# Performance work log

Measured on AMD Instinct MI355X. Metric: run time of the kernel, lower is better.

## Reference

```python
import jax, jax.numpy as jnp
import numpy as np

DIM = 768
N_HEADS = 12
HEAD_DIM = DIM // N_HEADS
B, S = 2, 2048


def fibonacci_mask(seq_len, causal=True):
    fibs = [1, 1]
    while fibs[-1] + fibs[-2] <= seq_len:
        fibs.append(fibs[-1] + fibs[-2])
    mask = np.zeros((seq_len, seq_len), dtype=bool)
    i = np.arange(seq_len)
    mask[i, i] = True  # self
    for f in fibs:
        rows = i[i - f >= 0]
        mask[rows, rows - f] = True
        if not causal:
            rows = i[i + f < seq_len]
            mask[rows, rows + f] = True
    return mask


def setup_inputs() -> dict:
    key = jax.random.key(0)
    k1, k2, k3, k4, k5 = jax.random.split(key, 5)
    x = jax.random.normal(k1, (B, S, DIM), dtype=jnp.float32)
    # Linear weights (torch layout: [out, in]), small init
    w_qkv = jax.random.normal(k2, (3 * DIM, DIM), dtype=jnp.float32) * (DIM ** -0.5)
    b_qkv = jax.random.normal(k3, (3 * DIM,), dtype=jnp.float32) * 0.02
    w_out = jax.random.normal(k4, (DIM, DIM), dtype=jnp.float32) * (DIM ** -0.5)
    b_out = jax.random.normal(k5, (DIM,), dtype=jnp.float32) * 0.02
    mask = jnp.asarray(fibonacci_mask(S, causal=True))  # [S,S] bool constant
    return {"x": x, "w_qkv": w_qkv, "b_qkv": b_qkv, "w_out": w_out, "b_out": b_out, "mask": mask}


def reference(x, w_qkv, b_qkv, w_out, b_out, mask):
    Bx, Sx, D = x.shape
    qkv = x @ w_qkv.T + b_qkv                                   # [B,S,3D]
    qkv = qkv.reshape(Bx, Sx, 3, N_HEADS, HEAD_DIM)
    qkv = jnp.transpose(qkv, (2, 0, 3, 1, 4))                   # [3,B,H,S,hd]
    q, k, v = qkv[0], qkv[1], qkv[2]
    scale = HEAD_DIM ** -0.5
    attn = jnp.einsum('bhqd,bhkd->bhqk', q, k) * scale          # [B,H,S,S]
    attn = jnp.where(mask[None, None], attn, -jnp.inf)
    attn = jax.nn.softmax(attn, axis=-1)
    attn = jnp.nan_to_num(attn, nan=0.0)
    out = jnp.einsum('bhqk,bhkd->bhqd', attn, v)                # [B,H,S,hd]
    out = jnp.transpose(out, (0, 2, 1, 3)).reshape(Bx, Sx, D)
    return out @ w_out.T + b_out
```

## Files before the change

kernel.cpp:

```cpp
#include <hip/hip_runtime.h>
#include <hip/hip_bf16.h>

#define DIM   768
#define NH    12
#define HD    64
#define BB    2
#define SS    2048
#define QKVN  (3 * DIM)
#define MM    (BB * SS)

typedef __attribute__((ext_vector_type(8))) short bf16x8;
typedef __attribute__((ext_vector_type(8))) short short8;
typedef __attribute__((ext_vector_type(4))) float f32x4;

__device__ __forceinline__ short f2bf(float f) {
    unsigned int u = __float_as_uint(f);
    unsigned int r = (u + 0x7FFFu + ((u >> 16) & 1u)) >> 16;
    return (short)r;
}
__device__ __forceinline__ float bf2f(short s) {
    return __uint_as_float((unsigned int)(unsigned short)s << 16);
}

__device__ __forceinline__ void gld16(const short* g, short* l) {
    __builtin_amdgcn_global_load_lds(
        (const __attribute__((address_space(1))) void*)g,
        (__attribute__((address_space(3))) void*)l, 16, 0, 0);
}

template<int N> __device__ __forceinline__ void waitvm() {
    if constexpr (N == 0) asm volatile("s_waitcnt vmcnt(0)" ::: "memory");
    else if constexpr (N == 3) asm volatile("s_waitcnt vmcnt(3)" ::: "memory");
    else if constexpr (N == 4) asm volatile("s_waitcnt vmcnt(4)" ::: "memory");
}

__global__ __launch_bounds__(256) void conv_kernel(
    const float* __restrict__ x,  short* __restrict__ xb,
    const float* __restrict__ wq, short* __restrict__ wqb,
    const float* __restrict__ wo, short* __restrict__ wob)
{
    const int nx = (MM * DIM) / 8;
    const int nq = (QKVN * DIM) / 8;
    int i8 = blockIdx.x * 256 + threadIdx.x;
    const float* src; short* dst;
    if (i8 < nx)           { src = x;  dst = xb; }
    else if (i8 < nx + nq) { i8 -= nx; src = wq; dst = wqb; }
    else                   { i8 -= nx + nq; src = wo; dst = wob; }
    const float4* p = (const float4*)src + (size_t)i8 * 2;
    float4 a = p[0], b = p[1];
    short8 r;
    r[0] = f2bf(a.x); r[1] = f2bf(a.y); r[2] = f2bf(a.z); r[3] = f2bf(a.w);
    r[4] = f2bf(b.x); r[5] = f2bf(b.y); r[6] = f2bf(b.z); r[7] = f2bf(b.w);
    *((short8*)dst + i8) = r;
}


template<int RT>
__device__ __forceinline__ void stage_op(const short* gb, int K, int k0, short* ld)
{
#pragma unroll
    for (int ii = 0; ii < RT / 64; ++ii)
        gld16(gb + (size_t)(64 * ii) * K + k0, ld + ii * 4096);
}

template<int MF, int NF>
__device__ __forceinline__ void read_frags(
    const short* lsA, const short* lsB, int arow, int brow, int kg, int sw,
    bf16x8 af[2][MF], bf16x8 bfr[2][NF])
{
#pragma unroll
    for (int kk = 0; kk < 2; ++kk) {
        const int ko = (kk * 32 + kg * 8) ^ sw;
#pragma unroll
        for (int i = 0; i < MF; ++i)
            af[kk][i] = *(const bf16x8*)&lsA[(arow + i * 16) * 64 + ko];
#pragma unroll
        for (int j = 0; j < NF; ++j)
            bfr[kk][j] = *(const bf16x8*)&lsB[(brow + j * 16) * 64 + ko];
    }
}

template<int MF, int NF>
__device__ __forceinline__ void mfma_frags(
    bf16x8 af[2][MF], bf16x8 bfr[2][NF], f32x4 acc[MF][NF])
{
#pragma unroll
    for (int kk = 0; kk < 2; ++kk)
#pragma unroll
        for (int i = 0; i < MF; ++i)
#pragma unroll
            for (int j = 0; j < NF; ++j)
                acc[i][j] = __builtin_amdgcn_mfma_f32_16x16x32_bf16(
                    af[kk][i], bfr[kk][j], acc[i][j], 0, 0, 0);
}

template<int MF, int NF, int ART, int BRT, int VC>
__device__ __forceinline__ void phase_steady(
    const short* lsA, const short* lsB, short* ldA, short* ldB,
    const short* Ab, const short* Bb, int K, int knext,
    int arow, int brow, int kg, int sw, f32x4 acc[MF][NF])
{
    bf16x8 af[2][MF], bfr[2][NF];
    read_frags<MF, NF>(lsA, lsB, arow, brow, kg, sw, af, bfr);
    asm volatile("s_waitcnt lgkmcnt(0)" ::: "memory");
    __builtin_amdgcn_s_barrier();
    stage_op<ART>(Ab, K, knext, ldA);
    stage_op<BRT>(Bb, K, knext, ldB);
    mfma_frags<MF, NF>(af, bfr, acc);
    waitvm<VC>();
    __builtin_amdgcn_s_barrier();
}

__global__ __launch_bounds__(512) void gemm_qkv_kernel(
    const short* __restrict__ A, const short* __restrict__ Bm,
    const float* __restrict__ bias, short* __restrict__ qkvh)
{
    constexpr int K = DIM, NT = 12;
    __shared__ short lsA0[8192], lsB0[8192], lsA1[8192], lsB1[8192];

    const int t    = threadIdx.x;
    const int lane = t & 63;
    const int wid  = t >> 6;
    const int wrow = wid >> 2, wcol = wid & 3;
    const int l16  = lane & 15;
    const int kg   = lane >> 4;
    const int row0 = blockIdx.y * 128;
    const int col0 = blockIdx.x * 128;

    const int srow = t >> 3;
    const int scol = ((t & 7) ^ (srow & 7)) * 8;
    const short* Ab = A  + (size_t)(row0 + srow) * K + scol;
    const short* Bb = Bm + (size_t)(col0 + srow) * K + scol;
    short* ldA0 = lsA0 + t * 8;  short* ldB0 = lsB0 + t * 8;
    short* ldA1 = lsA1 + t * 8;  short* ldB1 = lsB1 + t * 8;
    const int arow = wrow * 64 + l16;
    const int brow = wcol * 32 + l16;
    const int sw   = (l16 & 7) * 8;

    f32x4 acc[4][2];
#pragma unroll
    for (int i = 0; i < 4; ++i)
#pragma unroll
        for (int j = 0; j < 2; ++j) acc[i][j] = (f32x4){0.f, 0.f, 0.f, 0.f};

    stage_op<128>(Ab, K, 0, ldA0);
    stage_op<128>(Bb, K, 0, ldB0);
    stage_op<128>(Ab, K, 64, ldA1);
    stage_op<128>(Bb, K, 64, ldB1);
    waitvm<4>();
    __builtin_amdgcn_s_barrier();

#pragma unroll
    for (int kt = 0; kt < NT - 2; kt += 2) {
        phase_steady<4, 2, 128, 128, 4>(lsA0, lsB0, ldA0, ldB0, Ab, Bb, K,
                                        (kt + 2) * 64, arow, brow, kg, sw, acc);
        phase_steady<4, 2, 128, 128, 4>(lsA1, lsB1, ldA1, ldB1, Ab, Bb, K,
                                        (kt + 3) * 64, arow, brow, kg, sw, acc);
    }
    {
        bf16x8 af[2][4], bfr[2][2];
        read_frags<4, 2>(lsA0, lsB0, arow, brow, kg, sw, af, bfr);
        mfma_frags<4, 2>(af, bfr, acc);
        waitvm<0>();
        __builtin_amdgcn_s_barrier();
        read_frags<4, 2>(lsA1, lsB1, arow, brow, kg, sw, af, bfr);
        mfma_frags<4, 2>(af, bfr, acc);
    }

#pragma unroll
    for (int j = 0; j < 2; ++j) {
        const int col = col0 + wcol * 32 + j * 16 + l16;
        const int ty = col / DIM;
        const int hh = (col % DIM) >> 6;
        const int dd = col & 63;
        const float bv = bias[col];
        const size_t cbase = ((size_t)(ty * BB * NH) * SS) * HD;
#pragma unroll
        for (int i = 0; i < 4; ++i) {
            const int rbase = row0 + wrow * 64 + i * 16 + kg * 4;
#pragma unroll
            for (int r = 0; r < 4; ++r) {
                const int row = rbase + r;
                const int bq = row >> 11, sq = row & 2047;
                qkvh[cbase + (((size_t)(bq * NH + hh) * SS + sq) << 6) + dd] =
                    f2bf(acc[i][j][r] + bv);
            }
        }
    }
}

__global__ __launch_bounds__(512) void gemm_out_kernel(
    const short* __restrict__ A, const short* __restrict__ Bm,
    const float* __restrict__ bias, float* __restrict__ C)
{
    constexpr int K = DIM, N = DIM, NT = 12;
    __shared__ short lsA0[4096], lsB0[8192], lsA1[4096], lsB1[8192];

    const int t    = threadIdx.x;
    const int lane = t & 63;
    const int wid  = t >> 6;
    const int wrow = wid >> 2, wcol = wid & 3;
    const int l16  = lane & 15;
    const int kg   = lane >> 4;
    const int row0 = blockIdx.y * 64;
    const int col0 = blockIdx.x * 128;

    const int srow = t >> 3;
    const int scol = ((t & 7) ^ (srow & 7)) * 8;
    const short* Ab = A  + (size_t)(row0 + srow) * K + scol;
    const short* Bb = Bm + (size_t)(col0 + srow) * K + scol;
    short* ldA0 = lsA0 + t * 8;  short* ldB0 = lsB0 + t * 8;
    short* ldA1 = lsA1 + t * 8;  short* ldB1 = lsB1 + t * 8;
    const int arow = wrow * 32 + l16;
    const int brow = wcol * 32 + l16;
    const int sw   = (l16 & 7) * 8;

    f32x4 acc[2][2];
#pragma unroll
    for (int i = 0; i < 2; ++i)
#pragma unroll
        for (int j = 0; j < 2; ++j) acc[i][j] = (f32x4){0.f, 0.f, 0.f, 0.f};

    stage_op<64>(Ab, K, 0, ldA0);
    stage_op<128>(Bb, K, 0, ldB0);
    stage_op<64>(Ab, K, 64, ldA1);
    stage_op<128>(Bb, K, 64, ldB1);
    waitvm<3>();
    __builtin_amdgcn_s_barrier();

#pragma unroll
    for (int kt = 0; kt < NT - 2; kt += 2) {
        phase_steady<2, 2, 64, 128, 3>(lsA0, lsB0, ldA0, ldB0, Ab, Bb, K,
                                       (kt + 2) * 64, arow, brow, kg, sw, acc);
        phase_steady<2, 2, 64, 128, 3>(lsA1, lsB1, ldA1, ldB1, Ab, Bb, K,
                                       (kt + 3) * 64, arow, brow, kg, sw, acc);
    }
    {
        bf16x8 af[2][2], bfr[2][2];
        read_frags<2, 2>(lsA0, lsB0, arow, brow, kg, sw, af, bfr);
        mfma_frags<2, 2>(af, bfr, acc);
        waitvm<0>();
        __builtin_amdgcn_s_barrier();
        read_frags<2, 2>(lsA1, lsB1, arow, brow, kg, sw, af, bfr);
        mfma_frags<2, 2>(af, bfr, acc);
    }

#pragma unroll
    for (int j = 0; j < 2; ++j) {
        const int col = col0 + wcol * 32 + j * 16 + l16;
        const float bv = bias[col];
#pragma unroll
        for (int i = 0; i < 2; ++i) {
            const int rbase = row0 + wrow * 32 + i * 16 + kg * 4;
#pragma unroll
            for (int r = 0; r < 4; ++r)
                C[(size_t)(rbase + r) * N + col] = acc[i][j][r] + bv;
        }
    }
}

__global__ __launch_bounds__(256) void fib_attn_kernel(
    const short* __restrict__ qkvh, short* __restrict__ attn)
{
    const int idx   = blockIdx.x;
    const int j     = idx >> 3;
    const int bh    = (idx & 7) + 8 * (j >> 6);
    const int chunk = j & 63;
    const int wid   = threadIdx.x >> 6;
    const int lane  = threadIdx.x & 63;
    const int ql    = lane >> 3;
    const int c     = lane & 7;
    const int s     = chunk * 32 + wid * 8 + ql;
    const int b = bh / NH, h = bh % NH;

    constexpr size_t TYB = (size_t)BB * NH * SS * HD;
    const size_t base = ((size_t)bh * SS) << 6;
    const short* Kp = qkvh + TYB + base;
    const short* Vp = qkvh + 2 * TYB + base;

    float qv[8];
    {
        bf16x8 v = *(const bf16x8*)(qkvh + base + ((size_t)s << 6) + c * 8);
#pragma unroll
        for (int e = 0; e < 8; ++e) qv[e] = bf2f(v[e]);
    }

    constexpr int NF = 17;
    const int fib[NF] = {0, 1, 2, 3, 5, 8, 13, 21, 34, 55, 89, 144,
                         233, 377, 610, 987, 1597};
    float sc[NF];
#pragma unroll
    for (int f = 0; f < NF; ++f) {
        const bool ok = (fib[f] <= s);
        const int sk = ok ? s - fib[f] : s;
        bf16x8 kv = *(const bf16x8*)(Kp + ((size_t)sk << 6) + c * 8);
        float part = 0.f;
#pragma unroll
        for (int e = 0; e < 8; ++e) part += qv[e] * bf2f(kv[e]);
        part += __shfl_xor(part, 1, 64);
        part += __shfl_xor(part, 2, 64);
        part += __shfl_xor(part, 4, 64);
        sc[f] = ok ? part * 0.125f : -1e30f;
    }

    float mx = sc[0];
#pragma unroll
    for (int f = 1; f < NF; ++f) mx = fmaxf(mx, sc[f]);
    float den = 0.f;
#pragma unroll
    for (int f = 0; f < NF; ++f) { sc[f] = __expf(sc[f] - mx); den += sc[f]; }

    float o[8];
#pragma unroll
    for (int e = 0; e < 8; ++e) o[e] = 0.f;
#pragma unroll
    for (int f = 0; f < NF; ++f) {
        const int sk = (fib[f] <= s) ? s - fib[f] : s;
        bf16x8 vv = *(const bf16x8*)(Vp + ((size_t)sk << 6) + c * 8);
        const float w = sc[f];
#pragma unroll
        for (int e = 0; e < 8; ++e) o[e] += w * bf2f(vv[e]);
    }

    const float inv = 1.f / den;
    short8 r;
#pragma unroll
    for (int e = 0; e < 8; ++e) r[e] = f2bf(o[e] * inv);
    *(short8*)(attn + (size_t)(b * SS + s) * DIM + h * HD + c * 8) = r;
}

extern "C" void kernel_launch(void* const* d_in, const int* in_sizes, int n_in,
                              void* d_out, int out_size, void* d_ws, size_t ws_size,
                              hipStream_t stream)
{
    const float* x     = (const float*)d_in[0];
    const float* w_qkv = (const float*)d_in[1];
    const float* b_qkv = (const float*)d_in[2];
    const float* w_out = (const float*)d_in[3];
    const float* b_out = (const float*)d_in[4];
    float* out = (float*)d_out;

    short* qkvh  = (short*)d_ws;
    short* attnb = (short*)((char*)d_ws + 18874368);
    short* xb    = (short*)((char*)d_ws + 25165824);
    short* wqkvb = (short*)((char*)d_ws + 31457280);
    short* woutb = (short*)((char*)d_ws + 34996224);

    conv_kernel<<<dim3(2688, 1, 1), dim3(256, 1, 1), 0, stream>>>(
        x, xb, w_qkv, wqkvb, w_out, woutb);

    gemm_qkv_kernel<<<dim3(QKVN / 128, MM / 128, 1), dim3(512, 1, 1), 0, stream>>>(
        xb, wqkvb, b_qkv, qkvh);

    fib_attn_kernel<<<dim3(1536, 1, 1), dim3(256, 1, 1), 0, stream>>>(qkvh, attnb);

    gemm_out_kernel<<<dim3(DIM / 128, MM / 64, 1), dim3(512, 1, 1), 0, stream>>>(
        attnb, woutb, b_out, out);
}
```

Before: 59.47 us.

## Fuse fp32-to-bf16 conversion into GEMM loaders and remap block order

Removes the separate conversion kernel. Both GEMMs now load fp32 x and weights directly through registers and convert them with packed bf16 conversion instructions before writing to swizzled LDS, with loads issued one stage ahead. Block indices are remapped to 1D with a grouped ordering, likely to improve L2 reuse. This saves a launch and the bf16 intermediate round-trip, but doubles the global bytes read per GEMM tile and adds register pressure and VALU work in the main loop.

```diff
diff --git a/kernel.cpp b/kernel.cpp
--- a/kernel.cpp
+++ b/kernel.cpp
@@ -22,6 +22,18 @@
     return __uint_as_float((unsigned int)(unsigned short)s << 16);
 }
 
+__device__ __forceinline__ unsigned cvtpk(float lo, float hi) {
+    unsigned r;
+    asm("v_cvt_pk_bf16_f32 %0, %1, %2" : "=v"(r) : "v"(lo), "v"(hi));
+    return r;
+}
+__device__ __forceinline__ void wr16(short* dst, float4 a, float4 b) {
+    int4 v;
+    v.x = (int)cvtpk(a.x, a.y); v.y = (int)cvtpk(a.z, a.w);
+    v.z = (int)cvtpk(b.x, b.y); v.w = (int)cvtpk(b.z, b.w);
+    *(int4*)dst = v;
+}
+
 __device__ __forceinline__ void gld16(const short* g, short* l) {
     __builtin_amdgcn_global_load_lds(
         (const __attribute__((address_space(1))) void*)g,
@@ -30,28 +42,9 @@
 
 template<int N> __device__ __forceinline__ void waitvm() {
     if constexpr (N == 0) asm volatile("s_waitcnt vmcnt(0)" ::: "memory");
-    else if constexpr (N == 3) asm volatile("s_waitcnt vmcnt(3)" ::: "memory");
     else if constexpr (N == 4) asm volatile("s_waitcnt vmcnt(4)" ::: "memory");
-}
-
-__global__ __launch_bounds__(256) void conv_kernel(
-    const float* __restrict__ x,  short* __restrict__ xb,
-    const float* __restrict__ wq, short* __restrict__ wqb,
-    const float* __restrict__ wo, short* __restrict__ wob)
-{
-    const int nx = (MM * DIM) / 8;
-    const int nq = (QKVN * DIM) / 8;
-    int i8 = blockIdx.x * 256 + threadIdx.x;
-    const float* src; short* dst;
-    if (i8 < nx)           { src = x;  dst = xb; }
-    else if (i8 < nx + nq) { i8 -= nx; src = wq; dst = wqb; }
-    else                   { i8 -= nx + nq; src = wo; dst = wob; }
-    const float4* p = (const float4*)src + (size_t)i8 * 2;
-    float4 a = p[0], b = p[1];
-    short8 r;
-    r[0] = f2bf(a.x); r[1] = f2bf(a.y); r[2] = f2bf(a.z); r[3] = f2bf(a.w);
-    r[4] = f2bf(b.x); r[5] = f2bf(b.y); r[6] = f2bf(b.z); r[7] = f2bf(b.w);
-    *((short8*)dst + i8) = r;
+    else if constexpr (N == 5) asm volatile("s_waitcnt vmcnt(5)" ::: "memory");
+    else if constexpr (N == 8) asm volatile("s_waitcnt vmcnt(8)" ::: "memory");
 }
 
 
@@ -94,25 +87,37 @@
                     af[kk][i], bfr[kk][j], acc[i][j], 0, 0, 0);
 }
 
-template<int MF, int NF, int ART, int BRT, int VC>
-__device__ __forceinline__ void phase_steady(
-    const short* lsA, const short* lsB, short* ldA, short* ldB,
-    const short* Ab, const short* Bb, int K, int knext,
-    int arow, int brow, int kg, int sw, f32x4 acc[MF][NF])
-{
-    bf16x8 af[2][MF], bfr[2][NF];
-    read_frags<MF, NF>(lsA, lsB, arow, brow, kg, sw, af, bfr);
-    asm volatile("s_waitcnt lgkmcnt(0)" ::: "memory");
-    __builtin_amdgcn_s_barrier();
-    stage_op<ART>(Ab, K, knext, ldA);
-    stage_op<BRT>(Bb, K, knext, ldB);
-    mfma_frags<MF, NF>(af, bfr, acc);
-    waitvm<VC>();
+template<bool ISSUE, bool WRITE, int VC>
+__device__ __forceinline__ void g1_phase(
+    const short* lsRA, const short* lsRB, short* lsWA, short* lsWB,
+    const float* Ag, const float* Bg, int knext,
+    float4* sI, const float4* sW, int wr0, int wr1,
+    int arow, int brow, int kg, int sw, f32x4 acc[4][2])
+{
+    bf16x8 af[2][4], bfr[2][2];
+    read_frags<4, 2>(lsRA, lsRB, arow, brow, kg, sw, af, bfr);
+    asm volatile("s_waitcnt lgkmcnt(0)" ::: "memory");
+    __builtin_amdgcn_s_barrier();
+    if (ISSUE) {
+#pragma unroll
+        for (int w = 0; w < 4; ++w) sI[w]     = *(const float4*)(Ag + knext + w * 4);
+#pragma unroll
+        for (int w = 0; w < 4; ++w) sI[4 + w] = *(const float4*)(Bg + knext + w * 4);
+    }
+    if (WRITE) {
+        waitvm<VC>();
+        wr16((short*)lsWA + wr0, sW[0], sW[1]);
+        wr16((short*)lsWA + wr1, sW[2], sW[3]);
+        wr16((short*)lsWB + wr0, sW[4], sW[5]);
+        wr16((short*)lsWB + wr1, sW[6], sW[7]);
+    }
+    mfma_frags<4, 2>(af, bfr, acc);
+    asm volatile("s_waitcnt lgkmcnt(0)" ::: "memory");
     __builtin_amdgcn_s_barrier();
 }
 
 __global__ __launch_bounds__(512) void gemm_qkv_kernel(
-    const short* __restrict__ A, const short* __restrict__ Bm,
+    const float* __restrict__ A, const float* __restrict__ Bm,
     const float* __restrict__ bias, short* __restrict__ qkvh)
 {
     constexpr int K = DIM, NT = 12;
@@ -124,15 +129,19 @@
     const int wrow = wid >> 2, wcol = wid & 3;
     const int l16  = lane & 15;
     const int kg   = lane >> 4;
-    const int row0 = blockIdx.y * 128;
-    const int col0 = blockIdx.x * 128;
-
-    const int srow = t >> 3;
-    const int scol = ((t & 7) ^ (srow & 7)) * 8;
-    const short* Ab = A  + (size_t)(row0 + srow) * K + scol;
-    const short* Bb = Bm + (size_t)(col0 + srow) * K + scol;
-    short* ldA0 = lsA0 + t * 8;  short* ldB0 = lsB0 + t * 8;
-    short* ldA1 = lsA1 + t * 8;  short* ldB1 = lsB1 + t * 8;
+
+    const int bid = blockIdx.x;
+    const int jj  = bid >> 3;
+    const int row0 = ((bid & 7) * 4 + jj / 18) * 128;
+    const int col0 = (jj % 18) * 128;
+
+    const int srow = t >> 2;
+    const int sc4  = (t & 3) * 16;
+    const float* Ag = A  + (size_t)(row0 + srow) * K + sc4;
+    const float* Bg = Bm + (size_t)(col0 + srow) * K + sc4;
+    const int wr0 = srow * 64 + ((((t & 3) * 2 + 0) ^ (srow & 7)) * 8);
+    const int wr1 = srow * 64 + ((((t & 3) * 2 + 1) ^ (srow & 7)) * 8);
+
     const int arow = wrow * 64 + l16;
     const int brow = wcol * 32 + l16;
     const int sw   = (l16 & 7) * 8;
@@ -143,26 +152,34 @@
 #pragma unroll
         for (int j = 0; j < 2; ++j) acc[i][j] = (f32x4){0.f, 0.f, 0.f, 0.f};
 
-    stage_op<128>(Ab, K, 0, ldA0);
-    stage_op<128>(Bb, K, 0, ldB0);
-    stage_op<128>(Ab, K, 64, ldA1);
-    stage_op<128>(Bb, K, 64, ldB1);
-    waitvm<4>();
-    __builtin_amdgcn_s_barrier();
-
-#pragma unroll
-    for (int kt = 0; kt < NT - 2; kt += 2) {
-        phase_steady<4, 2, 128, 128, 4>(lsA0, lsB0, ldA0, ldB0, Ab, Bb, K,
-                                        (kt + 2) * 64, arow, brow, kg, sw, acc);
-        phase_steady<4, 2, 128, 128, 4>(lsA1, lsB1, ldA1, ldB1, Ab, Bb, K,
-                                        (kt + 3) * 64, arow, brow, kg, sw, acc);
-    }
+    float4 s0[8], s1[8];
+#pragma unroll
+    for (int w = 0; w < 4; ++w) s0[w]     = *(const float4*)(Ag + 0 + w * 4);
+#pragma unroll
+    for (int w = 0; w < 4; ++w) s0[4 + w] = *(const float4*)(Bg + 0 + w * 4);
+#pragma unroll
+    for (int w = 0; w < 4; ++w) s1[w]     = *(const float4*)(Ag + 64 + w * 4);
+#pragma unroll
+    for (int w = 0; w < 4; ++w) s1[4 + w] = *(const float4*)(Bg + 64 + w * 4);
+    waitvm<8>();
+    wr16(lsA0 + wr0, s0[0], s0[1]);
+    wr16(lsA0 + wr1, s0[2], s0[3]);
+    wr16(lsB0 + wr0, s0[4], s0[5]);
+    wr16(lsB0 + wr1, s0[6], s0[7]);
+    asm volatile("s_waitcnt lgkmcnt(0)" ::: "memory");
+    __builtin_amdgcn_s_barrier();
+
+#pragma unroll
+    for (int kt = 0; kt < 10; kt += 2) {
+        g1_phase<true, true, 8>(lsA0, lsB0, lsA1, lsB1, Ag, Bg, (kt + 2) * 64,
+                                s0, s1, wr0, wr1, arow, brow, kg, sw, acc);
+        g1_phase<true, true, 8>(lsA1, lsB1, lsA0, lsB0, Ag, Bg, (kt + 3) * 64,
+                                s1, s0, wr0, wr1, arow, brow, kg, sw, acc);
+    }
+    g1_phase<false, true, 0>(lsA0, lsB0, lsA1, lsB1, Ag, Bg, 0,
+                             s0, s1, wr0, wr1, arow, brow, kg, sw, acc);
     {
         bf16x8 af[2][4], bfr[2][2];
-        read_frags<4, 2>(lsA0, lsB0, arow, brow, kg, sw, af, bfr);
-        mfma_frags<4, 2>(af, bfr, acc);
-        waitvm<0>();
-        __builtin_amdgcn_s_barrier();
         read_frags<4, 2>(lsA1, lsB1, arow, brow, kg, sw, af, bfr);
         mfma_frags<4, 2>(af, bfr, acc);
     }
@@ -189,11 +206,37 @@
     }
 }
 
+template<bool ISSUE, bool WRITE, int VC>
+__device__ __forceinline__ void g2_phase(
+    const short* lsRA, const short* lsRB, short* lsWB,
+    const short* Agb, const float* Bg, int knext, short* ldA,
+    float4* sI, const float4* sW, int wr0, int wr1,
+    int arow, int brow, int kg, int sw, f32x4 acc[2][2])
+{
+    bf16x8 af[2][2], bfr[2][2];
+    read_frags<2, 2>(lsRA, lsRB, arow, brow, kg, sw, af, bfr);
+    asm volatile("s_waitcnt lgkmcnt(0)" ::: "memory");
+    __builtin_amdgcn_s_barrier();
+    if (ISSUE) {
+        stage_op<64>(Agb, DIM, knext, ldA);
+#pragma unroll
+        for (int w = 0; w < 4; ++w) sI[w] = *(const float4*)(Bg + knext + w * 4);
+    }
+    if (WRITE) {
+        waitvm<VC>();
+        wr16((short*)lsWB + wr0, sW[0], sW[1]);
+        wr16((short*)lsWB + wr1, sW[2], sW[3]);
+    }
+    mfma_frags<2, 2>(af, bfr, acc);
+    asm volatile("s_waitcnt lgkmcnt(0)" ::: "memory");
+    __builtin_amdgcn_s_barrier();
+}
+
 __global__ __launch_bounds__(512) void gemm_out_kernel(
-    const short* __restrict__ A, const short* __restrict__ Bm,
+    const short* __restrict__ A, const float* __restrict__ Bm,
     const float* __restrict__ bias, float* __restrict__ C)
 {
-    constexpr int K = DIM, N = DIM, NT = 12;
+    constexpr int K = DIM, N = DIM;
     __shared__ short lsA0[4096], lsB0[8192], lsA1[4096], lsB1[8192];
 
     const int t    = threadIdx.x;
@@ -202,15 +245,24 @@
     const int wrow = wid >> 2, wcol = wid & 3;
     const int l16  = lane & 15;
     const int kg   = lane >> 4;
-    const int row0 = blockIdx.y * 64;
-    const int col0 = blockIdx.x * 128;
-
-    const int srow = t >> 3;
-    const int scol = ((t & 7) ^ (srow & 7)) * 8;
-    const short* Ab = A  + (size_t)(row0 + srow) * K + scol;
-    const short* Bb = Bm + (size_t)(col0 + srow) * K + scol;
-    short* ldA0 = lsA0 + t * 8;  short* ldB0 = lsB0 + t * 8;
-    short* ldA1 = lsA1 + t * 8;  short* ldB1 = lsB1 + t * 8;
+
+    const int bid = blockIdx.x;
+    const int jj  = bid >> 3;
+    const int row0 = ((bid & 7) * 8 + jj / 6) * 64;
+    const int col0 = (jj % 6) * 128;
+
+    const int sra  = t >> 3;
+    const int scaa = ((t & 7) ^ (sra & 7)) * 8;
+    const short* Agb = A + (size_t)(row0 + sra) * K + scaa;
+    short* ldA0 = lsA0 + t * 8;
+    short* ldA1 = lsA1 + t * 8;
+
+    const int srow = t >> 2;
+    const int sc4  = (t & 3) * 16;
+    const float* Bg = Bm + (size_t)(col0 + srow) * K + sc4;
+    const int wr0 = srow * 64 + ((((t & 3) * 2 + 0) ^ (srow & 7)) * 8);
+    const int wr1 = srow * 64 + ((((t & 3) * 2 + 1) ^ (srow & 7)) * 8);
+
     const int arow = wrow * 32 + l16;
     const int brow = wcol * 32 + l16;
     const int sw   = (l16 & 7) * 8;
@@ -221,26 +273,30 @@
 #pragma unroll
         for (int j = 0; j < 2; ++j) acc[i][j] = (f32x4){0.f, 0.f, 0.f, 0.f};
 
-    stage_op<64>(Ab, K, 0, ldA0);
-    stage_op<128>(Bb, K, 0, ldB0);
-    stage_op<64>(Ab, K, 64, ldA1);
-    stage_op<128>(Bb, K, 64, ldB1);
-    waitvm<3>();
-    __builtin_amdgcn_s_barrier();
-
-#pragma unroll
-    for (int kt = 0; kt < NT - 2; kt += 2) {
-        phase_steady<2, 2, 64, 128, 3>(lsA0, lsB0, ldA0, ldB0, Ab, Bb, K,
-                                       (kt + 2) * 64, arow, brow, kg, sw, acc);
-        phase_steady<2, 2, 64, 128, 3>(lsA1, lsB1, ldA1, ldB1, Ab, Bb, K,
-                                       (kt + 3) * 64, arow, brow, kg, sw, acc);
-    }
+    float4 s0[4], s1[4];
+    stage_op<64>(Agb, K, 0, ldA0);
+    stage_op<64>(Agb, K, 64, ldA1);
+#pragma unroll
+    for (int w = 0; w < 4; ++w) s0[w] = *(const float4*)(Bg + 0 + w * 4);
+#pragma unroll
+    for (int w = 0; w < 4; ++w) s1[w] = *(const float4*)(Bg + 64 + w * 4);
+    waitvm<4>();
+    wr16(lsB0 + wr0, s0[0], s0[1]);
+    wr16(lsB0 + wr1, s0[2], s0[3]);
+    asm volatile("s_waitcnt lgkmcnt(0)" ::: "memory");
+    __builtin_amdgcn_s_barrier();
+
+#pragma unroll
+    for (int kt = 0; kt < 10; kt += 2) {
+        g2_phase<true, true, 5>(lsA0, lsB0, lsB1, Agb, Bg, (kt + 2) * 64, ldA0,
+                                s0, s1, wr0, wr1, arow, brow, kg, sw, acc);
+        g2_phase<true, true, 5>(lsA1, lsB1, lsB0, Agb, Bg, (kt + 3) * 64, ldA1,
+                                s1, s0, wr0, wr1, arow, brow, kg, sw, acc);
+    }
+    g2_phase<false, true, 0>(lsA0, lsB0, lsB1, Agb, Bg, 0, ldA0,
+                             s0, s1, wr0, wr1, arow, brow, kg, sw, acc);
     {
         bf16x8 af[2][2], bfr[2][2];
-        read_frags<2, 2>(lsA0, lsB0, arow, brow, kg, sw, af, bfr);
-        mfma_frags<2, 2>(af, bfr, acc);
-        waitvm<0>();
-        __builtin_amdgcn_s_barrier();
         read_frags<2, 2>(lsA1, lsB1, arow, brow, kg, sw, af, bfr);
         mfma_frags<2, 2>(af, bfr, acc);
     }
@@ -342,18 +398,12 @@
 
     short* qkvh  = (short*)d_ws;
     short* attnb = (short*)((char*)d_ws + 18874368);
-    short* xb    = (short*)((char*)d_ws + 25165824);
-    short* wqkvb = (short*)((char*)d_ws + 31457280);
-    short* woutb = (short*)((char*)d_ws + 34996224);
-
-    conv_kernel<<<dim3(2688, 1, 1), dim3(256, 1, 1), 0, stream>>>(
-        x, xb, w_qkv, wqkvb, w_out, woutb);
-
-    gemm_qkv_kernel<<<dim3(QKVN / 128, MM / 128, 1), dim3(512, 1, 1), 0, stream>>>(
-        xb, wqkvb, b_qkv, qkvh);
+
+    gemm_qkv_kernel<<<dim3(576, 1, 1), dim3(512, 1, 1), 0, stream>>>(
+        x, w_qkv, b_qkv, qkvh);
 
     fib_attn_kernel<<<dim3(1536, 1, 1), dim3(256, 1, 1), 0, stream>>>(qkvh, attnb);
 
-    gemm_out_kernel<<<dim3(DIM / 128, MM / 64, 1), dim3(512, 1, 1), 0, stream>>>(
-        attnb, woutb, b_out, out);
-}
+    gemm_out_kernel<<<dim3(384, 1, 1), dim3(512, 1, 1), 0, stream>>>(
+        attnb, w_out, b_out, out);
+}
```

Measured after the change: 83.12 us. 39.8% more time.

## Fuse fp32-to-bf16 conversion of x into QKV GEMM A-tile staging

Applied to the files above, without the earlier changes.

The QKV GEMM now reads x in fp32 directly through registers and converts it to bf16 with packed cvt instructions before writing swizzled LDS, so the separate conversion pass over x and its bf16 round trip through memory are removed. The weight conversion kernel now handles only the weights. The grid is flattened to 1D with a remapped block order for locality, and launch bounds are tightened. The cost is doubled global read bytes for A inside the GEMM and a register-staged pipeline that may expose more latency.

```diff
diff --git a/kernel.cpp b/kernel.cpp
--- a/kernel.cpp
+++ b/kernel.cpp
@@ -22,6 +22,18 @@
     return __uint_as_float((unsigned int)(unsigned short)s << 16);
 }
 
+__device__ __forceinline__ unsigned cvtpk(float lo, float hi) {
+    unsigned r;
+    asm("v_cvt_pk_bf16_f32 %0, %1, %2" : "=v"(r) : "v"(lo), "v"(hi));
+    return r;
+}
+__device__ __forceinline__ void wr16(short* dst, float4 a, float4 b) {
+    int4 v;
+    v.x = (int)cvtpk(a.x, a.y); v.y = (int)cvtpk(a.z, a.w);
+    v.z = (int)cvtpk(b.x, b.y); v.w = (int)cvtpk(b.z, b.w);
+    *(int4*)dst = v;
+}
+
 __device__ __forceinline__ void gld16(const short* g, short* l) {
     __builtin_amdgcn_global_load_lds(
         (const __attribute__((address_space(1))) void*)g,
@@ -32,20 +44,19 @@
     if constexpr (N == 0) asm volatile("s_waitcnt vmcnt(0)" ::: "memory");
     else if constexpr (N == 3) asm volatile("s_waitcnt vmcnt(3)" ::: "memory");
     else if constexpr (N == 4) asm volatile("s_waitcnt vmcnt(4)" ::: "memory");
-}
-
-__global__ __launch_bounds__(256) void conv_kernel(
-    const float* __restrict__ x,  short* __restrict__ xb,
+    else if constexpr (N == 6) asm volatile("s_waitcnt vmcnt(6)" ::: "memory");
+    else if constexpr (N == 8) asm volatile("s_waitcnt vmcnt(8)" ::: "memory");
+}
+
+__global__ __launch_bounds__(256) void conv_w_kernel(
     const float* __restrict__ wq, short* __restrict__ wqb,
     const float* __restrict__ wo, short* __restrict__ wob)
 {
-    const int nx = (MM * DIM) / 8;
     const int nq = (QKVN * DIM) / 8;
     int i8 = blockIdx.x * 256 + threadIdx.x;
     const float* src; short* dst;
-    if (i8 < nx)           { src = x;  dst = xb; }
-    else if (i8 < nx + nq) { i8 -= nx; src = wq; dst = wqb; }
-    else                   { i8 -= nx + nq; src = wo; dst = wob; }
+    if (i8 < nq) { src = wq; dst = wqb; }
+    else         { i8 -= nq; src = wo; dst = wob; }
     const float4* p = (const float4*)src + (size_t)i8 * 2;
     float4 a = p[0], b = p[1];
     short8 r;
@@ -111,11 +122,31 @@
     __builtin_amdgcn_s_barrier();
 }
 
-__global__ __launch_bounds__(512) void gemm_qkv_kernel(
-    const short* __restrict__ A, const short* __restrict__ Bm,
+#define G1_STEADY(lsRA, lsRB, LDB, lsWA, I, W, KN)                           \
+    {                                                                         \
+        bf16x8 af[2][4], bfr[2][2];                                           \
+        read_frags<4, 2>(lsRA, lsRB, arow, brow, kg, sw, af, bfr);            \
+        asm volatile("s_waitcnt lgkmcnt(0)" ::: "memory");                    \
+        __builtin_amdgcn_s_barrier();                                         \
+        I##0 = *(const float4*)(Ag + (KN));                                   \
+        I##1 = *(const float4*)(Ag + (KN) + 4);                               \
+        I##2 = *(const float4*)(Ag + (KN) + 8);                               \
+        I##3 = *(const float4*)(Ag + (KN) + 12);                              \
+        stage_op<128>(Bb, DIM, (KN), LDB);                                    \
+        waitvm<8>();                                                          \
+        wr16(lsWA + wr0, W##0, W##1);                                         \
+        wr16(lsWA + wr1, W##2, W##3);                                         \
+        mfma_frags<4, 2>(af, bfr, acc);                                       \
+        waitvm<6>();                                                          \
+        asm volatile("s_waitcnt lgkmcnt(0)" ::: "memory");                    \
+        __builtin_amdgcn_s_barrier();                                         \
+    }
+
+__global__ __launch_bounds__(512, 4) void gemm_qkv_kernel(
+    const float* __restrict__ A, const short* __restrict__ Bm,
     const float* __restrict__ bias, short* __restrict__ qkvh)
 {
-    constexpr int K = DIM, NT = 12;
+    constexpr int K = DIM;
     __shared__ short lsA0[8192], lsB0[8192], lsA1[8192], lsB1[8192];
 
     const int t    = threadIdx.x;
@@ -124,15 +155,22 @@
     const int wrow = wid >> 2, wcol = wid & 3;
     const int l16  = lane & 15;
     const int kg   = lane >> 4;
-    const int row0 = blockIdx.y * 128;
-    const int col0 = blockIdx.x * 128;
-
-    const int srow = t >> 3;
-    const int scol = ((t & 7) ^ (srow & 7)) * 8;
-    const short* Ab = A  + (size_t)(row0 + srow) * K + scol;
-    const short* Bb = Bm + (size_t)(col0 + srow) * K + scol;
-    short* ldA0 = lsA0 + t * 8;  short* ldB0 = lsB0 + t * 8;
-    short* ldA1 = lsA1 + t * 8;  short* ldB1 = lsB1 + t * 8;
+
+    const int bid = blockIdx.x;
+    const int jj  = bid >> 3;
+    const int row0 = ((bid & 7) * 4 + jj / 18) * 128;
+    const int col0 = (jj % 18) * 128;
+
+    const int srow = t >> 2;
+    const float* Ag = A + (size_t)(row0 + srow) * K + (t & 3) * 16;
+    const int wr0 = srow * 64 + ((((t & 3) * 2 + 0) ^ (srow & 7)) * 8);
+    const int wr1 = srow * 64 + ((((t & 3) * 2 + 1) ^ (srow & 7)) * 8);
+
+    const int srb = t >> 3;
+    const short* Bb = Bm + (size_t)(col0 + srb) * K + ((t & 7) ^ (srb & 7)) * 8;
+    short* ldB0 = lsB0 + t * 8;
+    short* ldB1 = lsB1 + t * 8;
+
     const int arow = wrow * 64 + l16;
     const int brow = wcol * 32 + l16;
     const int sw   = (l16 & 7) * 8;
@@ -143,26 +181,39 @@
 #pragma unroll
         for (int j = 0; j < 2; ++j) acc[i][j] = (f32x4){0.f, 0.f, 0.f, 0.f};
 
-    stage_op<128>(Ab, K, 0, ldA0);
-    stage_op<128>(Bb, K, 0, ldB0);
-    stage_op<128>(Ab, K, 64, ldA1);
-    stage_op<128>(Bb, K, 64, ldB1);
-    waitvm<4>();
+    float4 aP0, aP1, aP2, aP3, aQ0, aQ1, aQ2, aQ3;
+
+    aP0 = *(const float4*)(Ag);      aP1 = *(const float4*)(Ag + 4);
+    aP2 = *(const float4*)(Ag + 8);  aP3 = *(const float4*)(Ag + 12);
+    stage_op<128>(Bb, DIM, 0, ldB0);
+    aQ0 = *(const float4*)(Ag + 64); aQ1 = *(const float4*)(Ag + 68);
+    aQ2 = *(const float4*)(Ag + 72); aQ3 = *(const float4*)(Ag + 76);
+    stage_op<128>(Bb, DIM, 64, ldB1);
+    waitvm<8>();
+    wr16(lsA0 + wr0, aP0, aP1);
+    wr16(lsA0 + wr1, aP2, aP3);
+    waitvm<6>();
+    asm volatile("s_waitcnt lgkmcnt(0)" ::: "memory");
     __builtin_amdgcn_s_barrier();
 
-#pragma unroll
-    for (int kt = 0; kt < NT - 2; kt += 2) {
-        phase_steady<4, 2, 128, 128, 4>(lsA0, lsB0, ldA0, ldB0, Ab, Bb, K,
-                                        (kt + 2) * 64, arow, brow, kg, sw, acc);
-        phase_steady<4, 2, 128, 128, 4>(lsA1, lsB1, ldA1, ldB1, Ab, Bb, K,
-                                        (kt + 3) * 64, arow, brow, kg, sw, acc);
+    for (int kt = 0; kt < 10; kt += 2) {
+        G1_STEADY(lsA0, lsB0, ldB0, lsA1, aP, aQ, (kt + 2) * 64)
+        G1_STEADY(lsA1, lsB1, ldB1, lsA0, aQ, aP, (kt + 3) * 64)
     }
     {
         bf16x8 af[2][4], bfr[2][2];
         read_frags<4, 2>(lsA0, lsB0, arow, brow, kg, sw, af, bfr);
+        asm volatile("s_waitcnt lgkmcnt(0)" ::: "memory");
+        __builtin_amdgcn_s_barrier();
+        waitvm<0>();
+        wr16(lsA1 + wr0, aQ0, aQ1);
+        wr16(lsA1 + wr1, aQ2, aQ3);
         mfma_frags<4, 2>(af, bfr, acc);
-        waitvm<0>();
+        asm volatile("s_waitcnt lgkmcnt(0)" ::: "memory");
         __builtin_amdgcn_s_barrier();
+    }
+    {
+        bf16x8 af[2][4], bfr[2][2];
         read_frags<4, 2>(lsA1, lsB1, arow, brow, kg, sw, af, bfr);
         mfma_frags<4, 2>(af, bfr, acc);
     }
@@ -342,18 +393,17 @@
 
     short* qkvh  = (short*)d_ws;
     short* attnb = (short*)((char*)d_ws + 18874368);
-    short* xb    = (short*)((char*)d_ws + 25165824);
-    short* wqkvb = (short*)((char*)d_ws + 31457280);
-    short* woutb = (short*)((char*)d_ws + 34996224);
-
-    conv_kernel<<<dim3(2688, 1, 1), dim3(256, 1, 1), 0, stream>>>(
-        x, xb, w_qkv, wqkvb, w_out, woutb);
-
-    gemm_qkv_kernel<<<dim3(QKVN / 128, MM / 128, 1), dim3(512, 1, 1), 0, stream>>>(
-        xb, wqkvb, b_qkv, qkvh);
+    short* wqkvb = (short*)((char*)d_ws + 25165824);
+    short* woutb = (short*)((char*)d_ws + 28704768);
+
+    conv_w_kernel<<<dim3(1152, 1, 1), dim3(256, 1, 1), 0, stream>>>(
+        w_qkv, wqkvb, w_out, woutb);
+
+    gemm_qkv_kernel<<<dim3(576, 1, 1), dim3(512, 1, 1), 0, stream>>>(
+        x, wqkvb, b_qkv, qkvh);
 
     fib_attn_kernel<<<dim3(1536, 1, 1), dim3(256, 1, 1), 0, stream>>>(qkvh, attnb);
 
-    gemm_out_kernel<<<dim3(DIM / 128, MM / 64, 1), dim3(512, 1, 1), 0, stream>>>(
+    gemm_out_kernel<<<dim3(6, 64, 1), dim3(512, 1, 1), 0, stream>>>(
         attnb, woutb, b_out, out);
 }
```

Result: slower. 70.12 us (+17.9%).
